# Optimization experiments

Hardware: AMD Instinct MI355X
Metric: run time of the kernel (lower is better)

The kernel has to match this reference:

```python
import jax, jax.numpy as jnp
import numpy as np

B, S, H = 2, 2048, 2048
NH = 16
Q_LORA, KV_LORA = 1536, 512
D_NOPE, D_ROPE, D_V = 128, 64, 128
D_QK = D_NOPE + D_ROPE
SCALE = 1.0 / np.sqrt(D_QK)
EPS = 1e-6


def _freqs(seq_len):
    # precompute_freqs_cis with scaling_factor=1.0 -> plain RoPE
    inv = 1.0 / (10000.0 ** (np.arange(0, D_ROPE, 2, dtype=np.float32) / D_ROPE))
    t = np.arange(seq_len, dtype=np.float32)
    f = np.outer(t, inv)  # (S, D_ROPE//2)
    return jnp.asarray(np.cos(f)), jnp.asarray(np.sin(f))


def _rope_interleaved(x, cos, sin):
    # x: (B, S, heads, D_ROPE); cos/sin: (S, D_ROPE//2)
    b, s, h, d = x.shape
    xr = x.reshape(b, s, h, d // 2, 2)
    e, o = xr[..., 0], xr[..., 1]
    c = cos[None, :, None, :]
    sn = sin[None, :, None, :]
    re = e * c - o * sn
    im = e * sn + o * c
    return jnp.stack([re, im], axis=-1).reshape(b, s, h, d)


def _rmsnorm(x, w):
    xf = x.astype(jnp.float32)
    rms = jnp.sqrt(jnp.mean(xf * xf, axis=-1, keepdims=True) + EPS)
    return (w * (xf / rms)).astype(x.dtype)


def setup_inputs() -> dict:
    key = jax.random.key(0)
    ks = jax.random.split(key, 6)
    def w(k, shape, fan_in):
        return jax.random.normal(k, shape, dtype=jnp.float32) * (1.0 / np.sqrt(fan_in))
    return {
        "hidden_states": jax.random.normal(ks[0], (B, S, H), dtype=jnp.float32),
        "wq_a": w(ks[1], (Q_LORA, H), H),
        "q_norm_w": jnp.ones((Q_LORA,), dtype=jnp.float32),
        "wq_b": w(ks[2], (NH * D_QK, Q_LORA), Q_LORA),
        "wkv_a": w(ks[3], (KV_LORA + D_ROPE, H), H),
        "kv_norm_w": jnp.ones((KV_LORA,), dtype=jnp.float32),
        "wkv_b": w(ks[4], (NH * (D_NOPE + D_V), KV_LORA), KV_LORA),
        "wo": w(ks[5], (H, NH * D_V), NH * D_V),
    }


def reference(hidden_states, wq_a, q_norm_w, wq_b, wkv_a, kv_norm_w, wkv_b, wo):
    b, s, _ = hidden_states.shape
    cos, sin = _freqs(s)

    # low-rank Q path
    q = hidden_states @ wq_a.T                      # (B,S,Q_LORA)
    q = _rmsnorm(q, q_norm_w)
    q = (q @ wq_b.T).reshape(b, s, NH, D_QK)        # (B,S,NH,192)
    q_nope, q_pe = q[..., :D_NOPE], q[..., D_NOPE:]

    # joint KV compression
    kv = hidden_states @ wkv_a.T                    # (B,S,KV_LORA+D_ROPE)
    kv_c, k_pe = kv[..., :KV_LORA], kv[..., KV_LORA:]
    kv_c = _rmsnorm(kv_c, kv_norm_w)
    k_pe = _rope_interleaved(k_pe[:, :, None, :], cos, sin)  # (B,S,1,64)

    kv_x = (kv_c @ wkv_b.T).reshape(b, s, NH, D_NOPE + D_V)
    k_nope, v = kv_x[..., :D_NOPE], kv_x[..., D_NOPE:]

    q_pe = _rope_interleaved(q_pe, cos, sin)
    qf = jnp.concatenate([q_nope, q_pe], axis=-1)   # (B,S,NH,192)
    kf = jnp.concatenate([k_nope, jnp.broadcast_to(k_pe, (b, s, NH, D_ROPE))], axis=-1)

    scores = jnp.einsum("bqhd,bkhd->bhqk", qf, kf) * SCALE
    attn = jax.nn.softmax(scores.astype(jnp.float32), axis=-1).astype(qf.dtype)
    out = jnp.einsum("bhqk,bkhd->bqhd", attn, v).reshape(b, s, NH * D_V)
    return out @ wo.T
```

## Files before the change

### kernel.cpp

```cpp
#include <hip/hip_runtime.h>
#include <math.h>

#define B_   2
#define S_   2048
#define H_   2048
#define NH_  16
#define T_   (B_*S_)
#define QL   1536
#define KVL  512
#define DN   128
#define DR   64
#define DQK  192
#define DV   128
#define SCALE_ 0.07216878364870323f
#define EPS_ 1e-6f

typedef unsigned short u16;
typedef __attribute__((ext_vector_type(8))) short bf16x8;
typedef __attribute__((ext_vector_type(4))) float f32x4;

__device__ __forceinline__ u16 f2b(float x) {
  union { float f; unsigned u; } v; v.f = x;
  unsigned r = v.u + 0x7FFFu + ((v.u >> 16) & 1u);
  return (u16)(r >> 16);
}
__device__ __forceinline__ float b2f(u16 u) {
  union { unsigned u; float f; } v; v.u = ((unsigned)u) << 16; return v.f;
}

#define GLD16(src, dst) __builtin_amdgcn_global_load_lds(                       \
    (const __attribute__((address_space(1))) unsigned int*)(src),               \
    (__attribute__((address_space(3))) unsigned int*)(dst), 16, 0, 0)

__global__ __launch_bounds__(256) void cvt_bf16(const float* __restrict__ in,
                                                u16* __restrict__ out, int n4) {
  int i = blockIdx.x * 256 + threadIdx.x;
  if (i >= n4) return;
  float4 v = ((const float4*)in)[i];
  u16 r[4] = {f2b(v.x), f2b(v.y), f2b(v.z), f2b(v.w)};
  ((uint2*)out)[i] = *(uint2*)r;
}

__global__ __launch_bounds__(256) void cvt_wkva(const float* __restrict__ in,
                                                u16* __restrict__ out) {
  int i = blockIdx.x * 256 + threadIdx.x;
  if (i >= 640 * 512) return;
  int row = i >> 9;
  u16 r[4] = {0, 0, 0, 0};
  if (row < 576) {
    float4 v = ((const float4*)in)[i];
    r[0] = f2b(v.x); r[1] = f2b(v.y); r[2] = f2b(v.z); r[3] = f2b(v.w);
  }
  ((uint2*)out)[i] = *(uint2*)r;
}

template <int OUTMODE>
__global__ __launch_bounds__(256) void gemm_mfma(
    const u16* __restrict__ A, int lda,
    const u16* __restrict__ W, int ldw,
    float* __restrict__ Cf, u16* __restrict__ Cb, int ldc,
    int K, float outscale) {
  __shared__ u16 As[4096];
  __shared__ u16 Bs[4096];
  const int tid = threadIdx.x;
  const int wave = tid >> 6, lane = tid & 63, quad = lane >> 4, l16 = lane & 15;
  const int wm = (wave >> 1) * 64, wn = (wave & 1) * 64;
  const size_t m0 = (size_t)blockIdx.y * 128, n0 = (size_t)blockIdx.x * 128;

  f32x4 acc[4][4];
#pragma unroll
  for (int i = 0; i < 4; ++i)
#pragma unroll
    for (int j = 0; j < 4; ++j) acc[i][j] = (f32x4){0.f, 0.f, 0.f, 0.f};

  const int g0 = tid, g1 = tid + 256;
  const u16* a0 = A + (m0 + (g0 >> 6) * 16 + (g0 & 15)) * (size_t)lda + ((g0 >> 4) & 3) * 8;
  const u16* a1 = A + (m0 + (g1 >> 6) * 16 + (g1 & 15)) * (size_t)lda + ((g1 >> 4) & 3) * 8;
  const u16* b0 = W + (n0 + (g0 >> 6) * 16 + (g0 & 15)) * (size_t)ldw + ((g0 >> 4) & 3) * 8;
  const u16* b1 = W + (n0 + (g1 >> 6) * 16 + (g1 & 15)) * (size_t)ldw + ((g1 >> 4) & 3) * 8;

  for (int k0 = 0; k0 < K; k0 += 32) {
    __syncthreads();
    GLD16(a0 + k0, &As[g0 * 8]);
    GLD16(a1 + k0, &As[g1 * 8]);
    GLD16(b0 + k0, &Bs[g0 * 8]);
    GLD16(b1 + k0, &Bs[g1 * 8]);
    __syncthreads();

    bf16x8 af[4], bfr[4];
#pragma unroll
    for (int i = 0; i < 4; ++i)
      af[i] = *(const bf16x8*)&As[((wm >> 4) + i) * 512 + quad * 128 + l16 * 8];
#pragma unroll
    for (int j = 0; j < 4; ++j)
      bfr[j] = *(const bf16x8*)&Bs[((wn >> 4) + j) * 512 + quad * 128 + l16 * 8];
#pragma unroll
    for (int i = 0; i < 4; ++i)
#pragma unroll
      for (int j = 0; j < 4; ++j)
        acc[i][j] = __builtin_amdgcn_mfma_f32_16x16x32_bf16(af[i], bfr[j], acc[i][j], 0, 0, 0);
  }

#pragma unroll
  for (int i = 0; i < 4; ++i)
#pragma unroll
    for (int j = 0; j < 4; ++j)
#pragma unroll
      for (int r = 0; r < 4; ++r) {
        size_t m = m0 + wm + i * 16 + quad * 4 + r;
        size_t n = n0 + wn + j * 16 + l16;
        if (OUTMODE == 0) Cf[m * ldc + n] = acc[i][j][r];
        else              Cb[m * ldc + n] = f2b(acc[i][j][r] * outscale);
      }
}

__global__ __launch_bounds__(256) void rmsnorm_bf(
    const float* __restrict__ x, const float* __restrict__ w,
    u16* __restrict__ o, int D, int sx, int so) {
  const float* p = x + (size_t)blockIdx.x * sx;
  u16* q = o + (size_t)blockIdx.x * so;
  float ss = 0.f;
  for (int i = threadIdx.x; i < D; i += 256) { float v = p[i]; ss += v * v; }
#pragma unroll
  for (int off = 32; off; off >>= 1) ss += __shfl_down(ss, off);
  __shared__ float red[4];
  __shared__ float s_inv;
  if ((threadIdx.x & 63) == 0) red[threadIdx.x >> 6] = ss;
  __syncthreads();
  if (threadIdx.x == 0) {
    float t = red[0] + red[1] + red[2] + red[3];
    s_inv = 1.0f / sqrtf(t / (float)D + EPS_);
  }
  __syncthreads();
  float inv = s_inv;
  for (int i = threadIdx.x; i < D; i += 256) q[i] = f2b(w[i] * p[i] * inv);
}

__global__ void rope_q_bf(u16* __restrict__ Q) {
  int idx = blockIdx.x * blockDim.x + threadIdx.x;
  int pair = idx & 31;
  int head = (idx >> 5) & (NH_ - 1);
  int row = idx >> 9;
  if (row >= T_) return;
  int s = row & (S_ - 1);
  float inv = powf(10000.0f, -(float)(2 * pair) * (1.0f / 64.0f));
  float ang = (float)s * inv;
  float c = cosf(ang), sn = sinf(ang);
  u16* p = Q + (size_t)row * (NH_ * DQK) + head * DQK + DN + 2 * pair;
  unsigned u = *(unsigned*)p;
  float e = b2f((u16)(u & 0xffff)), o = b2f((u16)(u >> 16));
  float re = e * c - o * sn;
  float im = e * sn + o * c;
  *(unsigned*)p = (unsigned)f2b(re) | ((unsigned)f2b(im) << 16);
}

__global__ void kpe_bf_kernel(const float* __restrict__ KVa, u16* __restrict__ KPE) {
  int idx = blockIdx.x * blockDim.x + threadIdx.x;
  int pair = idx & 31;
  int row = idx >> 5;
  if (row >= T_) return;
  int s = row & (S_ - 1);
  float inv = powf(10000.0f, -(float)(2 * pair) * (1.0f / 64.0f));
  float ang = (float)s * inv;
  float c = cosf(ang), sn = sinf(ang);
  const float* p = KVa + (size_t)row * 640 + KVL + 2 * pair;
  float e = p[0], o = p[1];
  float re = e * c - o * sn;
  float im = e * sn + o * c;
  *(unsigned*)(KPE + (size_t)row * 64 + 2 * pair) =
      (unsigned)f2b(re) | ((unsigned)f2b(im) << 16);
}

__global__ __launch_bounds__(256) void conv_vt(const u16* __restrict__ KVbf,
                                               u16* __restrict__ Vt) {
  const int h = blockIdx.y, b = blockIdx.z;
  const int s0 = (blockIdx.x >> 1) * 64, d0 = (blockIdx.x & 1) * 64;
  const int t0 = b * S_;
  __shared__ u16 tile[64][72];
  const int tid = threadIdx.x;
#pragma unroll
  for (int i = 0; i < 2; ++i) {
    int c = tid + i * 256;
    int row = c >> 3, off = (c & 7) * 8;
    *(uint4*)&tile[row][off] =
        *(const uint4*)(KVbf + (size_t)(t0 + s0 + row) * 4096 + h * 256 + 128 + d0 + off);
  }
  __syncthreads();
#pragma unroll
  for (int i = 0; i < 2; ++i) {
    int c = tid + i * 256;
    int drow = c >> 3, soff = (c & 7) * 8;
    u16 vals[8];
#pragma unroll
    for (int j = 0; j < 8; ++j) vals[j] = tile[soff + j][drow];
    *(uint4*)(Vt + ((size_t)(b * NH_ + h) * 128 + d0 + drow) * 2048 + s0 + soff) =
        *(uint4*)vals;
  }
}

__global__ __launch_bounds__(256) void flash_mfma(
    const u16* __restrict__ Qbf,
    const u16* __restrict__ KVbf,
    const u16* __restrict__ KPE,
    const u16* __restrict__ Vt,
    u16* __restrict__ Out) {
  const int h = blockIdx.y, b = blockIdx.z;
  const int q0 = blockIdx.x * 64;
  const int t0 = b * S_;
  const int tid = threadIdx.x;
  const int wave = tid >> 6, lane = tid & 63, quad = lane >> 4, l16 = lane & 15;

  __shared__ u16 Ks[64][200];
  __shared__ u16 Vs[128][72];
  __shared__ u16 Ps[4][16][72];

  bf16x8 qf[6];
  {
    const u16* qp = Qbf + (size_t)(t0 + q0 + wave * 16 + l16) * (NH_ * DQK) + h * DQK + quad * 8;
#pragma unroll
    for (int c = 0; c < 6; ++c) qf[c] = *(const bf16x8*)(qp + c * 32);
  }

  f32x4 of[8];
#pragma unroll
  for (int i = 0; i < 8; ++i) of[i] = (f32x4){0.f, 0.f, 0.f, 0.f};
  float mrun[4] = {-3e38f, -3e38f, -3e38f, -3e38f};
  float lrun[4] = {0.f, 0.f, 0.f, 0.f};

  for (int kt = 0; kt < S_; kt += 64) {
    __syncthreads();
#pragma unroll
    for (int i = 0; i < 6; ++i) {
      int c = tid + i * 256;
      int row = c / 24, off = c % 24;
      const u16* src = (off < 16)
          ? KVbf + (size_t)(t0 + kt + row) * 4096 + h * 256 + off * 8
          : KPE + (size_t)(t0 + kt + row) * 64 + (off - 16) * 8;
      *(uint4*)&Ks[row][off * 8] = *(const uint4*)src;
    }
#pragma unroll
    for (int i = 0; i < 4; ++i) {
      int c = tid + i * 256;
      int row = c >> 3, off = (c & 7) * 8;
      *(uint4*)&Vs[row][off] =
          *(const uint4*)(Vt + ((size_t)(b * NH_ + h) * 128 + row) * 2048 + kt + off);
    }
    __syncthreads();

    f32x4 sc[4];
#pragma unroll
    for (int kk = 0; kk < 4; ++kk) {
      f32x4 s = (f32x4){0.f, 0.f, 0.f, 0.f};
#pragma unroll
      for (int c = 0; c < 6; ++c) {
        bf16x8 kf = *(const bf16x8*)&Ks[kk * 16 + l16][quad * 8 + c * 32];
        s = __builtin_amdgcn_mfma_f32_16x16x32_bf16(qf[c], kf, s, 0, 0, 0);
      }
      sc[kk] = s;
    }
    float tm[4];
#pragma unroll
    for (int r = 0; r < 4; ++r)
      tm[r] = fmaxf(fmaxf(sc[0][r], sc[1][r]), fmaxf(sc[2][r], sc[3][r]));
#pragma unroll
    for (int off = 1; off < 16; off <<= 1)
#pragma unroll
      for (int r = 0; r < 4; ++r) tm[r] = fmaxf(tm[r], __shfl_xor(tm[r], off, 64));
    float alpha[4], rs[4], p[4][4];
#pragma unroll
    for (int r = 0; r < 4; ++r) {
      float mnew = fmaxf(mrun[r], tm[r]);
      alpha[r] = __expf(mrun[r] - mnew);
      mrun[r] = mnew;
      float s0 = 0.f;
#pragma unroll
      for (int kk = 0; kk < 4; ++kk) {
        float pv = __expf(sc[kk][r] - mnew);
        p[kk][r] = pv;
        s0 += pv;
      }
      rs[r] = s0;
    }
#pragma unroll
    for (int off = 1; off < 16; off <<= 1)
#pragma unroll
      for (int r = 0; r < 4; ++r) rs[r] += __shfl_xor(rs[r], off, 64);
#pragma unroll
    for (int r = 0; r < 4; ++r) lrun[r] = lrun[r] * alpha[r] + rs[r];

#pragma unroll
    for (int kk = 0; kk < 4; ++kk)
#pragma unroll
      for (int r = 0; r < 4; ++r)
        Ps[wave][quad * 4 + r][kk * 16 + l16] = f2b(p[kk][r]);

#pragma unroll
    for (int dt = 0; dt < 8; ++dt)
#pragma unroll
      for (int r = 0; r < 4; ++r) of[dt][r] *= alpha[r];

    bf16x8 pa0 = *(const bf16x8*)&Ps[wave][l16][quad * 8];
    bf16x8 pa1 = *(const bf16x8*)&Ps[wave][l16][32 + quad * 8];
#pragma unroll
    for (int dt = 0; dt < 8; ++dt) {
      bf16x8 v0 = *(const bf16x8*)&Vs[dt * 16 + l16][quad * 8];
      bf16x8 v1 = *(const bf16x8*)&Vs[dt * 16 + l16][32 + quad * 8];
      of[dt] = __builtin_amdgcn_mfma_f32_16x16x32_bf16(pa0, v0, of[dt], 0, 0, 0);
      of[dt] = __builtin_amdgcn_mfma_f32_16x16x32_bf16(pa1, v1, of[dt], 0, 0, 0);
    }
  }

#pragma unroll
  for (int r = 0; r < 4; ++r) {
    float inv = 1.0f / lrun[r];
    u16* op = Out + (size_t)(t0 + q0 + wave * 16 + quad * 4 + r) * (NH_ * DV) + h * DV + l16;
#pragma unroll
    for (int dt = 0; dt < 8; ++dt) op[dt * 16] = f2b(of[dt][r] * inv);
  }
}

extern "C" void kernel_launch(void* const* d_in, const int* in_sizes, int n_in,
                              void* d_out, int out_size, void* d_ws, size_t ws_size,
                              hipStream_t stream) {
  const float* hidden  = (const float*)d_in[0];
  const float* wq_a    = (const float*)d_in[1];
  const float* q_norm  = (const float*)d_in[2];
  const float* wq_b    = (const float*)d_in[3];
  const float* wkv_a   = (const float*)d_in[4];
  const float* kv_norm = (const float*)d_in[5];
  const float* wkv_b   = (const float*)d_in[6];
  const float* wo      = (const float*)d_in[7];
  float* out = (float*)d_out;

  float* ws = (float*)d_ws;
  u16*   hid_bf = (u16*)(ws);
  u16*   wbuf   = (u16*)(ws + 4194304);
  float* q_a    = ws + 6553600;
  u16*   vt     = (u16*)(ws + 6553600);
  u16*   kpe    = (u16*)(ws + 10747904);
  float* kv_a   = ws + 12845056;
  u16*   qn_bf  = (u16*)(ws + 15466496);
  u16*   attn_bf= (u16*)(ws + 15466496);
  u16*   q_bf   = (u16*)(ws + 19660800);
  u16*   kvn_bf = (u16*)(ws + 25952256);
  u16*   kv_bf  = (u16*)(ws + 27000832);
  const size_t need = (size_t)(27000832 + 8388608) * sizeof(float);
  if (ws_size < need) return;

  cvt_bf16<<<8192, 256, 0, stream>>>(hidden, hid_bf, 2097152);

  cvt_bf16<<<3072, 256, 0, stream>>>(wq_a, wbuf, 786432);
  gemm_mfma<0><<<dim3(QL / 128, T_ / 128), 256, 0, stream>>>(
      hid_bf, H_, wbuf, H_, q_a, nullptr, QL, H_, 1.0f);
  rmsnorm_bf<<<T_, 256, 0, stream>>>(q_a, q_norm, qn_bf, QL, QL, QL);
  cvt_bf16<<<4608, 256, 0, stream>>>(wq_b, wbuf, 1179648);
  gemm_mfma<1><<<dim3(NH_ * DQK / 128, T_ / 128), 256, 0, stream>>>(
      qn_bf, QL, wbuf, QL, nullptr, q_bf, NH_ * DQK, QL, SCALE_);
  rope_q_bf<<<T_ * NH_ * 32 / 256, 256, 0, stream>>>(q_bf);

  cvt_wkva<<<1280, 256, 0, stream>>>(wkv_a, wbuf);
  gemm_mfma<0><<<dim3(640 / 128, T_ / 128), 256, 0, stream>>>(
      hid_bf, H_, wbuf, H_, kv_a, nullptr, 640, H_, 1.0f);
  rmsnorm_bf<<<T_, 256, 0, stream>>>(kv_a, kv_norm, kvn_bf, KVL, 640, KVL);
  kpe_bf_kernel<<<T_ * 32 / 256, 256, 0, stream>>>(kv_a, kpe);
  cvt_bf16<<<2048, 256, 0, stream>>>(wkv_b, wbuf, 524288);
  gemm_mfma<1><<<dim3(NH_ * (DN + DV) / 128, T_ / 128), 256, 0, stream>>>(
      kvn_bf, KVL, wbuf, KVL, nullptr, kv_bf, NH_ * (DN + DV), KVL, 1.0f);
  conv_vt<<<dim3(64, NH_, B_), 256, 0, stream>>>(kv_bf, vt);

  flash_mfma<<<dim3(S_ / 64, NH_, B_), 256, 0, stream>>>(q_bf, kv_bf, kpe, vt, attn_bf);

  cvt_bf16<<<4096, 256, 0, stream>>>(wo, wbuf, 1048576);
  gemm_mfma<0><<<dim3(H_ / 128, T_ / 128), 256, 0, stream>>>(
      attn_bf, NH_ * DV, wbuf, NH_ * DV, out, nullptr, H_, NH_ * DV, 1.0f);
}
```

Baseline: 710.2 us.

## Process two query tiles per wave in flash attention with fragment-ordered LDS

Doubles the query rows per block to 128, so each wave handles two 16-row query tiles. Every K and V fragment read from LDS now feeds two MFMAs, which halves per-query K/V staging and LDS read traffic. K, V and P are stored in LDS in MFMA-fragment order rather than padded row-major, and the K/V global load addresses are computed once before the loop and advanced by a stride each iteration. The cost is more accumulator registers (launch bounds ask for 2 blocks per CU) and half as many blocks in the grid.

```diff
diff --git a/kernel.cpp b/kernel.cpp
--- a/kernel.cpp
+++ b/kernel.cpp
@@ -198,125 +198,153 @@
   }
 }
 
-__global__ __launch_bounds__(256) void flash_mfma(
+__global__ __launch_bounds__(256, 2) void flash_mfma(
     const u16* __restrict__ Qbf,
     const u16* __restrict__ KVbf,
     const u16* __restrict__ KPE,
     const u16* __restrict__ Vt,
     u16* __restrict__ Out) {
   const int h = blockIdx.y, b = blockIdx.z;
-  const int q0 = blockIdx.x * 64;
+  const int q0 = blockIdx.x * 128;
   const int t0 = b * S_;
   const int tid = threadIdx.x;
   const int wave = tid >> 6, lane = tid & 63, quad = lane >> 4, l16 = lane & 15;
-
-  __shared__ u16 Ks[64][200];
-  __shared__ u16 Vs[128][72];
-  __shared__ u16 Ps[4][16][72];
-
-  bf16x8 qf[6];
-  {
-    const u16* qp = Qbf + (size_t)(t0 + q0 + wave * 16 + l16) * (NH_ * DQK) + h * DQK + quad * 8;
-#pragma unroll
-    for (int c = 0; c < 6; ++c) qf[c] = *(const bf16x8*)(qp + c * 32);
-  }
-
-  f32x4 of[8];
-#pragma unroll
-  for (int i = 0; i < 8; ++i) of[i] = (f32x4){0.f, 0.f, 0.f, 0.f};
-  float mrun[4] = {-3e38f, -3e38f, -3e38f, -3e38f};
-  float lrun[4] = {0.f, 0.f, 0.f, 0.f};
+  const int wq = wave * 32;
+
+  __shared__ u16 Ks[64 * 192];
+  __shared__ u16 Vs[128 * 64];
+  __shared__ u16 Ps[4][2][16 * 64];
+
+  bf16x8 qf[2][6];
+#pragma unroll
+  for (int t = 0; t < 2; ++t) {
+    const u16* qp = Qbf + (size_t)(t0 + q0 + wq + t * 16 + l16) * (NH_ * DQK) + h * DQK + quad * 8;
+#pragma unroll
+    for (int c = 0; c < 6; ++c) qf[t][c] = *(const bf16x8*)(qp + c * 32);
+  }
+
+  const u16* kbase[6]; int kstep[6];
+#pragma unroll
+  for (int i = 0; i < 6; ++i) {
+    int g = i * 256 + tid;
+    int r = g & 15, cc = (g >> 4) % 24, kk = (g >> 4) / 24;
+    int tok = kk * 16 + r;
+    if (cc < 16) { kbase[i] = KVbf + (size_t)(t0 + tok) * 4096 + h * 256 + cc * 8; kstep[i] = 64 * 4096; }
+    else         { kbase[i] = KPE + (size_t)(t0 + tok) * 64 + (cc - 16) * 8;       kstep[i] = 64 * 64; }
+  }
+  const u16* vbase[4];
+#pragma unroll
+  for (int i = 0; i < 4; ++i) {
+    int g = i * 256 + tid;
+    int r = g & 15, kc = (g >> 4) & 7, dt = g >> 7;
+    vbase[i] = Vt + ((size_t)((b * NH_ + h) * 128) + dt * 16 + r) * 2048 + kc * 8;
+  }
+
+  f32x4 of[2][8];
+#pragma unroll
+  for (int t = 0; t < 2; ++t)
+#pragma unroll
+    for (int i = 0; i < 8; ++i) of[t][i] = (f32x4){0.f, 0.f, 0.f, 0.f};
+  float mrun[2][4], lrun[2][4];
+#pragma unroll
+  for (int t = 0; t < 2; ++t)
+#pragma unroll
+    for (int r = 0; r < 4; ++r) { mrun[t][r] = -3e38f; lrun[t][r] = 0.f; }
 
   for (int kt = 0; kt < S_; kt += 64) {
     __syncthreads();
 #pragma unroll
-    for (int i = 0; i < 6; ++i) {
-      int c = tid + i * 256;
-      int row = c / 24, off = c % 24;
-      const u16* src = (off < 16)
-          ? KVbf + (size_t)(t0 + kt + row) * 4096 + h * 256 + off * 8
-          : KPE + (size_t)(t0 + kt + row) * 64 + (off - 16) * 8;
-      *(uint4*)&Ks[row][off * 8] = *(const uint4*)src;
+    for (int i = 0; i < 6; ++i) GLD16(kbase[i], &Ks[(i * 256 + tid) * 8]);
+#pragma unroll
+    for (int i = 0; i < 4; ++i) GLD16(vbase[i] + kt, &Vs[(i * 256 + tid) * 8]);
+#pragma unroll
+    for (int i = 0; i < 6; ++i) kbase[i] += kstep[i];
+    __syncthreads();
+
+    f32x4 sc[2][4];
+#pragma unroll
+    for (int kk = 0; kk < 4; ++kk) {
+      sc[0][kk] = (f32x4){0.f, 0.f, 0.f, 0.f};
+      sc[1][kk] = (f32x4){0.f, 0.f, 0.f, 0.f};
+#pragma unroll
+      for (int c = 0; c < 6; ++c) {
+        bf16x8 kf = *(const bf16x8*)&Ks[(kk * 384 + (c * 4 + quad) * 16 + l16) * 8];
+        sc[0][kk] = __builtin_amdgcn_mfma_f32_16x16x32_bf16(qf[0][c], kf, sc[0][kk], 0, 0, 0);
+        sc[1][kk] = __builtin_amdgcn_mfma_f32_16x16x32_bf16(qf[1][c], kf, sc[1][kk], 0, 0, 0);
+      }
     }
-#pragma unroll
-    for (int i = 0; i < 4; ++i) {
-      int c = tid + i * 256;
-      int row = c >> 3, off = (c & 7) * 8;
-      *(uint4*)&Vs[row][off] =
-          *(const uint4*)(Vt + ((size_t)(b * NH_ + h) * 128 + row) * 2048 + kt + off);
+
+    float alpha[2][4];
+#pragma unroll
+    for (int t = 0; t < 2; ++t) {
+      float tm[4], rs[4];
+#pragma unroll
+      for (int r = 0; r < 4; ++r)
+        tm[r] = fmaxf(fmaxf(sc[t][0][r], sc[t][1][r]), fmaxf(sc[t][2][r], sc[t][3][r]));
+#pragma unroll
+      for (int off = 1; off < 16; off <<= 1)
+#pragma unroll
+        for (int r = 0; r < 4; ++r) tm[r] = fmaxf(tm[r], __shfl_xor(tm[r], off, 64));
+#pragma unroll
+      for (int r = 0; r < 4; ++r) {
+        float mnew = fmaxf(mrun[t][r], tm[r]);
+        alpha[t][r] = __expf(mrun[t][r] - mnew);
+        mrun[t][r] = mnew;
+        float s0 = 0.f;
+#pragma unroll
+        for (int kk = 0; kk < 4; ++kk) {
+          float pv = __expf(sc[t][kk][r] - mnew);
+          sc[t][kk][r] = pv;
+          s0 += pv;
+        }
+        rs[r] = s0;
+      }
+#pragma unroll
+      for (int off = 1; off < 16; off <<= 1)
+#pragma unroll
+        for (int r = 0; r < 4; ++r) rs[r] += __shfl_xor(rs[r], off, 64);
+#pragma unroll
+      for (int r = 0; r < 4; ++r) lrun[t][r] = lrun[t][r] * alpha[t][r] + rs[r];
+#pragma unroll
+      for (int kk = 0; kk < 4; ++kk)
+#pragma unroll
+        for (int r = 0; r < 4; ++r)
+          Ps[wave][t][((kk * 2 + (l16 >> 3)) * 16 + quad * 4 + r) * 8 + (l16 & 7)] =
+              f2b(sc[t][kk][r]);
     }
-    __syncthreads();
-
-    f32x4 sc[4];
-#pragma unroll
-    for (int kk = 0; kk < 4; ++kk) {
-      f32x4 s = (f32x4){0.f, 0.f, 0.f, 0.f};
-#pragma unroll
-      for (int c = 0; c < 6; ++c) {
-        bf16x8 kf = *(const bf16x8*)&Ks[kk * 16 + l16][quad * 8 + c * 32];
-        s = __builtin_amdgcn_mfma_f32_16x16x32_bf16(qf[c], kf, s, 0, 0, 0);
+
+    bf16x8 pa[2][2];
+#pragma unroll
+    for (int t = 0; t < 2; ++t)
+#pragma unroll
+      for (int c2 = 0; c2 < 2; ++c2)
+        pa[t][c2] = *(const bf16x8*)&Ps[wave][t][((c2 * 4 + quad) * 16 + l16) * 8];
+#pragma unroll
+    for (int t = 0; t < 2; ++t)
+#pragma unroll
+      for (int dt = 0; dt < 8; ++dt)
+#pragma unroll
+        for (int r = 0; r < 4; ++r) of[t][dt][r] *= alpha[t][r];
+#pragma unroll
+    for (int dt = 0; dt < 8; ++dt) {
+#pragma unroll
+      for (int c2 = 0; c2 < 2; ++c2) {
+        bf16x8 vf = *(const bf16x8*)&Vs[(dt * 128 + (c2 * 4 + quad) * 16 + l16) * 8];
+        of[0][dt] = __builtin_amdgcn_mfma_f32_16x16x32_bf16(pa[0][c2], vf, of[0][dt], 0, 0, 0);
+        of[1][dt] = __builtin_amdgcn_mfma_f32_16x16x32_bf16(pa[1][c2], vf, of[1][dt], 0, 0, 0);
       }
-      sc[kk] = s;
     }
-    float tm[4];
-#pragma unroll
-    for (int r = 0; r < 4; ++r)
-      tm[r] = fmaxf(fmaxf(sc[0][r], sc[1][r]), fmaxf(sc[2][r], sc[3][r]));
-#pragma unroll
-    for (int off = 1; off < 16; off <<= 1)
-#pragma unroll
-      for (int r = 0; r < 4; ++r) tm[r] = fmaxf(tm[r], __shfl_xor(tm[r], off, 64));
-    float alpha[4], rs[4], p[4][4];
+  }
+
+#pragma unroll
+  for (int t = 0; t < 2; ++t)
 #pragma unroll
     for (int r = 0; r < 4; ++r) {
-      float mnew = fmaxf(mrun[r], tm[r]);
-      alpha[r] = __expf(mrun[r] - mnew);
-      mrun[r] = mnew;
-      float s0 = 0.f;
-#pragma unroll
-      for (int kk = 0; kk < 4; ++kk) {
-        float pv = __expf(sc[kk][r] - mnew);
-        p[kk][r] = pv;
-        s0 += pv;
-      }
-      rs[r] = s0;
+      float inv = 1.0f / lrun[t][r];
+      u16* op = Out + (size_t)(t0 + q0 + wq + t * 16 + quad * 4 + r) * (NH_ * DV) + h * DV + l16;
+#pragma unroll
+      for (int dt = 0; dt < 8; ++dt) op[dt * 16] = f2b(of[t][dt][r] * inv);
     }
-#pragma unroll
-    for (int off = 1; off < 16; off <<= 1)
-#pragma unroll
-      for (int r = 0; r < 4; ++r) rs[r] += __shfl_xor(rs[r], off, 64);
-#pragma unroll
-    for (int r = 0; r < 4; ++r) lrun[r] = lrun[r] * alpha[r] + rs[r];
-
-#pragma unroll
-    for (int kk = 0; kk < 4; ++kk)
-#pragma unroll
-      for (int r = 0; r < 4; ++r)
-        Ps[wave][quad * 4 + r][kk * 16 + l16] = f2b(p[kk][r]);
-
-#pragma unroll
-    for (int dt = 0; dt < 8; ++dt)
-#pragma unroll
-      for (int r = 0; r < 4; ++r) of[dt][r] *= alpha[r];
-
-    bf16x8 pa0 = *(const bf16x8*)&Ps[wave][l16][quad * 8];
-    bf16x8 pa1 = *(const bf16x8*)&Ps[wave][l16][32 + quad * 8];
-#pragma unroll
-    for (int dt = 0; dt < 8; ++dt) {
-      bf16x8 v0 = *(const bf16x8*)&Vs[dt * 16 + l16][quad * 8];
-      bf16x8 v1 = *(const bf16x8*)&Vs[dt * 16 + l16][32 + quad * 8];
-      of[dt] = __builtin_amdgcn_mfma_f32_16x16x32_bf16(pa0, v0, of[dt], 0, 0, 0);
-      of[dt] = __builtin_amdgcn_mfma_f32_16x16x32_bf16(pa1, v1, of[dt], 0, 0, 0);
-    }
-  }
-
-#pragma unroll
-  for (int r = 0; r < 4; ++r) {
-    float inv = 1.0f / lrun[r];
-    u16* op = Out + (size_t)(t0 + q0 + wave * 16 + quad * 4 + r) * (NH_ * DV) + h * DV + l16;
-#pragma unroll
-    for (int dt = 0; dt < 8; ++dt) op[dt * 16] = f2b(of[dt][r] * inv);
-  }
 }
 
 extern "C" void kernel_launch(void* const* d_in, const int* in_sizes, int n_in,
@@ -368,7 +396,7 @@
       kvn_bf, KVL, wbuf, KVL, nullptr, kv_bf, NH_ * (DN + DV), KVL, 1.0f);
   conv_vt<<<dim3(64, NH_, B_), 256, 0, stream>>>(kv_bf, vt);
 
-  flash_mfma<<<dim3(S_ / 64, NH_, B_), 256, 0, stream>>>(q_bf, kv_bf, kpe, vt, attn_bf);
+  flash_mfma<<<dim3(S_ / 128, NH_, B_), 256, 0, stream>>>(q_bf, kv_bf, kpe, vt, attn_bf);
 
   cvt_bf16<<<4096, 256, 0, stream>>>(wo, wbuf, 1048576);
   gemm_mfma<0><<<dim3(H_ / 128, T_ / 128), 256, 0, stream>>>(
```

New measurement: 677.9 us. 1.05x faster.

## Fuse fp32-to-bf16 conversions and use async LDS loads in flash attention

Applied to the files above, without the earlier changes.

All six fp32-to-bf16 conversions are merged into one launch, and the workspace is reorganised so each converted weight gets its own buffer instead of sharing one. The flash attention kernel moves to 512-thread blocks covering 128 queries. K and V tiles are loaded with global_load_lds directly into a fragment-ordered LDS layout, and the P scratch reuses the K buffer behind an extra barrier. The aim is fewer launches, fewer K/V tile reloads per head, and cheaper tile staging. The cost is an added __syncthreads per iteration and a larger workspace.

```diff
diff --git a/kernel.cpp b/kernel.cpp
--- a/kernel.cpp
+++ b/kernel.cpp
@@ -32,26 +32,39 @@
     (const __attribute__((address_space(1))) unsigned int*)(src),               \
     (__attribute__((address_space(3))) unsigned int*)(dst), 16, 0, 0)
 
-__global__ __launch_bounds__(256) void cvt_bf16(const float* __restrict__ in,
-                                                u16* __restrict__ out, int n4) {
-  int i = blockIdx.x * 256 + threadIdx.x;
-  if (i >= n4) return;
+__device__ __forceinline__ void cvt4(const float* in, u16* out, int i) {
   float4 v = ((const float4*)in)[i];
   u16 r[4] = {f2b(v.x), f2b(v.y), f2b(v.z), f2b(v.w)};
   ((uint2*)out)[i] = *(uint2*)r;
 }
 
-__global__ __launch_bounds__(256) void cvt_wkva(const float* __restrict__ in,
-                                                u16* __restrict__ out) {
+__global__ __launch_bounds__(256) void cvt_all(
+    const float* __restrict__ hid, const float* __restrict__ wqa,
+    const float* __restrict__ wqb, const float* __restrict__ wkva,
+    const float* __restrict__ wkvb, const float* __restrict__ wo,
+    u16* __restrict__ o_hid, u16* __restrict__ o_wqa, u16* __restrict__ o_wqb,
+    u16* __restrict__ o_wkva, u16* __restrict__ o_wkvb, u16* __restrict__ o_wo) {
   int i = blockIdx.x * 256 + threadIdx.x;
-  if (i >= 640 * 512) return;
-  int row = i >> 9;
-  u16 r[4] = {0, 0, 0, 0};
-  if (row < 576) {
-    float4 v = ((const float4*)in)[i];
-    r[0] = f2b(v.x); r[1] = f2b(v.y); r[2] = f2b(v.z); r[3] = f2b(v.w);
-  }
-  ((uint2*)out)[i] = *(uint2*)r;
+  if (i < 2097152) { cvt4(hid, o_hid, i); return; }
+  i -= 2097152;
+  if (i < 786432) { cvt4(wqa, o_wqa, i); return; }
+  i -= 786432;
+  if (i < 1179648) { cvt4(wqb, o_wqb, i); return; }
+  i -= 1179648;
+  if (i < 327680) {
+    int row = i >> 9;
+    u16 r[4] = {0, 0, 0, 0};
+    if (row < 576) {
+      float4 v = ((const float4*)wkva)[i];
+      r[0] = f2b(v.x); r[1] = f2b(v.y); r[2] = f2b(v.z); r[3] = f2b(v.w);
+    }
+    ((uint2*)o_wkva)[i] = *(uint2*)r;
+    return;
+  }
+  i -= 327680;
+  if (i < 524288) { cvt4(wkvb, o_wkvb, i); return; }
+  i -= 524288;
+  if (i < 1048576) cvt4(wo, o_wo, i);
 }
 
 template <int OUTMODE>
@@ -198,21 +211,21 @@
   }
 }
 
-__global__ __launch_bounds__(256) void flash_mfma(
+__global__ __launch_bounds__(512, 4) void flash_mfma(
     const u16* __restrict__ Qbf,
     const u16* __restrict__ KVbf,
     const u16* __restrict__ KPE,
     const u16* __restrict__ Vt,
     u16* __restrict__ Out) {
   const int h = blockIdx.y, b = blockIdx.z;
-  const int q0 = blockIdx.x * 64;
+  const int q0 = blockIdx.x * 128;
   const int t0 = b * S_;
   const int tid = threadIdx.x;
   const int wave = tid >> 6, lane = tid & 63, quad = lane >> 4, l16 = lane & 15;
 
-  __shared__ u16 Ks[64][200];
-  __shared__ u16 Vs[128][72];
-  __shared__ u16 Ps[4][16][72];
+  __shared__ u16 Ks[64 * 192];
+  __shared__ u16 Vs[128 * 64];
+  u16* Ps = &Ks[wave * 1024];
 
   bf16x8 qf[6];
   {
@@ -221,6 +234,23 @@
     for (int c = 0; c < 6; ++c) qf[c] = *(const bf16x8*)(qp + c * 32);
   }
 
+  const u16* kbase[3]; int kstep[3];
+#pragma unroll
+  for (int i = 0; i < 3; ++i) {
+    int g = i * 512 + tid;
+    int r = g & 15, cc = (g >> 4) % 24, kk = (g >> 4) / 24;
+    int tok = kk * 16 + r;
+    if (cc < 16) { kbase[i] = KVbf + (size_t)(t0 + tok) * 4096 + h * 256 + cc * 8; kstep[i] = 64 * 4096; }
+    else         { kbase[i] = KPE + (size_t)(t0 + tok) * 64 + (cc - 16) * 8;       kstep[i] = 64 * 64; }
+  }
+  const u16* vbase[2];
+#pragma unroll
+  for (int i = 0; i < 2; ++i) {
+    int g = i * 512 + tid;
+    int r = g & 15, kc = (g >> 4) & 7, dt = g >> 7;
+    vbase[i] = Vt + ((size_t)((b * NH_ + h) * 128) + dt * 16 + r) * 2048 + kc * 8;
+  }
+
   f32x4 of[8];
 #pragma unroll
   for (int i = 0; i < 8; ++i) of[i] = (f32x4){0.f, 0.f, 0.f, 0.f};
@@ -230,21 +260,11 @@
   for (int kt = 0; kt < S_; kt += 64) {
     __syncthreads();
 #pragma unroll
-    for (int i = 0; i < 6; ++i) {
-      int c = tid + i * 256;
-      int row = c / 24, off = c % 24;
-      const u16* src = (off < 16)
-          ? KVbf + (size_t)(t0 + kt + row) * 4096 + h * 256 + off * 8
-          : KPE + (size_t)(t0 + kt + row) * 64 + (off - 16) * 8;
-      *(uint4*)&Ks[row][off * 8] = *(const uint4*)src;
-    }
-#pragma unroll
-    for (int i = 0; i < 4; ++i) {
-      int c = tid + i * 256;
-      int row = c >> 3, off = (c & 7) * 8;
-      *(uint4*)&Vs[row][off] =
-          *(const uint4*)(Vt + ((size_t)(b * NH_ + h) * 128 + row) * 2048 + kt + off);
-    }
+    for (int i = 0; i < 3; ++i) GLD16(kbase[i], &Ks[(i * 512 + tid) * 8]);
+#pragma unroll
+    for (int i = 0; i < 2; ++i) GLD16(vbase[i] + kt, &Vs[(i * 512 + tid) * 8]);
+#pragma unroll
+    for (int i = 0; i < 3; ++i) kbase[i] += kstep[i];
     __syncthreads();
 
     f32x4 sc[4];
@@ -253,12 +273,13 @@
       f32x4 s = (f32x4){0.f, 0.f, 0.f, 0.f};
 #pragma unroll
       for (int c = 0; c < 6; ++c) {
-        bf16x8 kf = *(const bf16x8*)&Ks[kk * 16 + l16][quad * 8 + c * 32];
+        bf16x8 kf = *(const bf16x8*)&Ks[((kk * 24 + c * 4 + quad) * 16 + l16) * 8];
         s = __builtin_amdgcn_mfma_f32_16x16x32_bf16(qf[c], kf, s, 0, 0, 0);
       }
       sc[kk] = s;
     }
-    float tm[4];
+
+    float tm[4], rs[4], alpha[4];
 #pragma unroll
     for (int r = 0; r < 4; ++r)
       tm[r] = fmaxf(fmaxf(sc[0][r], sc[1][r]), fmaxf(sc[2][r], sc[3][r]));
@@ -266,7 +287,6 @@
     for (int off = 1; off < 16; off <<= 1)
 #pragma unroll
       for (int r = 0; r < 4; ++r) tm[r] = fmaxf(tm[r], __shfl_xor(tm[r], off, 64));
-    float alpha[4], rs[4], p[4][4];
 #pragma unroll
     for (int r = 0; r < 4; ++r) {
       float mnew = fmaxf(mrun[r], tm[r]);
@@ -276,7 +296,7 @@
 #pragma unroll
       for (int kk = 0; kk < 4; ++kk) {
         float pv = __expf(sc[kk][r] - mnew);
-        p[kk][r] = pv;
+        sc[kk][r] = pv;
         s0 += pv;
       }
       rs[r] = s0;
@@ -288,25 +308,30 @@
 #pragma unroll
     for (int r = 0; r < 4; ++r) lrun[r] = lrun[r] * alpha[r] + rs[r];
 
+    __syncthreads();
+
 #pragma unroll
     for (int kk = 0; kk < 4; ++kk)
 #pragma unroll
       for (int r = 0; r < 4; ++r)
-        Ps[wave][quad * 4 + r][kk * 16 + l16] = f2b(p[kk][r]);
+        Ps[((kk * 2 + (l16 >> 3)) * 16 + quad * 4 + r) * 8 + (l16 & 7)] = f2b(sc[kk][r]);
 
 #pragma unroll
     for (int dt = 0; dt < 8; ++dt)
 #pragma unroll
       for (int r = 0; r < 4; ++r) of[dt][r] *= alpha[r];
 
-    bf16x8 pa0 = *(const bf16x8*)&Ps[wave][l16][quad * 8];
-    bf16x8 pa1 = *(const bf16x8*)&Ps[wave][l16][32 + quad * 8];
+    bf16x8 pa[2];
+#pragma unroll
+    for (int c2 = 0; c2 < 2; ++c2)
+      pa[c2] = *(const bf16x8*)&Ps[((c2 * 4 + quad) * 16 + l16) * 8];
 #pragma unroll
     for (int dt = 0; dt < 8; ++dt) {
-      bf16x8 v0 = *(const bf16x8*)&Vs[dt * 16 + l16][quad * 8];
-      bf16x8 v1 = *(const bf16x8*)&Vs[dt * 16 + l16][32 + quad * 8];
-      of[dt] = __builtin_amdgcn_mfma_f32_16x16x32_bf16(pa0, v0, of[dt], 0, 0, 0);
-      of[dt] = __builtin_amdgcn_mfma_f32_16x16x32_bf16(pa1, v1, of[dt], 0, 0, 0);
+#pragma unroll
+      for (int c2 = 0; c2 < 2; ++c2) {
+        bf16x8 vf = *(const bf16x8*)&Vs[((dt * 8 + c2 * 4 + quad) * 16 + l16) * 8];
+        of[dt] = __builtin_amdgcn_mfma_f32_16x16x32_bf16(pa[c2], vf, of[dt], 0, 0, 0);
+      }
     }
   }
 
@@ -333,44 +358,44 @@
   float* out = (float*)d_out;
 
   float* ws = (float*)d_ws;
-  u16*   hid_bf = (u16*)(ws);
-  u16*   wbuf   = (u16*)(ws + 4194304);
-  float* q_a    = ws + 6553600;
-  u16*   vt     = (u16*)(ws + 6553600);
-  u16*   kpe    = (u16*)(ws + 10747904);
-  float* kv_a   = ws + 12845056;
-  u16*   qn_bf  = (u16*)(ws + 15466496);
-  u16*   attn_bf= (u16*)(ws + 15466496);
-  u16*   q_bf   = (u16*)(ws + 19660800);
-  u16*   kvn_bf = (u16*)(ws + 25952256);
-  u16*   kv_bf  = (u16*)(ws + 27000832);
-  const size_t need = (size_t)(27000832 + 8388608) * sizeof(float);
+  u16*   hid_bf  = (u16*)(ws);
+  u16*   wqa_bf  = (u16*)(ws + 4194304);
+  u16*   wqb_bf  = (u16*)(ws + 5767168);
+  u16*   wkva_bf = (u16*)(ws + 8126464);
+  u16*   wkvb_bf = (u16*)(ws + 8781824);
+  u16*   wo_bf   = (u16*)(ws + 9830400);
+  float* q_a     = ws + 11927552;
+  u16*   attn_bf = (u16*)(ws + 11927552);
+  u16*   qn_bf   = (u16*)(ws + 18219008);
+  u16*   vt      = (u16*)(ws + 18219008);
+  float* kv_a    = ws + 19791872;
+  u16*   q_bf    = (u16*)(ws + 22413312);
+  u16*   kvn_bf  = (u16*)(ws + 28704768);
+  u16*   kpe     = (u16*)(ws + 29753344);
+  u16*   kv_bf   = (u16*)(ws + 29884416);
+  const size_t need = (size_t)38273024 * sizeof(float);
   if (ws_size < need) return;
 
-  cvt_bf16<<<8192, 256, 0, stream>>>(hidden, hid_bf, 2097152);
-
-  cvt_bf16<<<3072, 256, 0, stream>>>(wq_a, wbuf, 786432);
+  cvt_all<<<23296, 256, 0, stream>>>(hidden, wq_a, wq_b, wkv_a, wkv_b, wo,
+                                     hid_bf, wqa_bf, wqb_bf, wkva_bf, wkvb_bf, wo_bf);
+
   gemm_mfma<0><<<dim3(QL / 128, T_ / 128), 256, 0, stream>>>(
-      hid_bf, H_, wbuf, H_, q_a, nullptr, QL, H_, 1.0f);
+      hid_bf, H_, wqa_bf, H_, q_a, nullptr, QL, H_, 1.0f);
   rmsnorm_bf<<<T_, 256, 0, stream>>>(q_a, q_norm, qn_bf, QL, QL, QL);
-  cvt_bf16<<<4608, 256, 0, stream>>>(wq_b, wbuf, 1179648);
   gemm_mfma<1><<<dim3(NH_ * DQK / 128, T_ / 128), 256, 0, stream>>>(
-      qn_bf, QL, wbuf, QL, nullptr, q_bf, NH_ * DQK, QL, SCALE_);
+      qn_bf, QL, wqb_bf, QL, nullptr, q_bf, NH_ * DQK, QL, SCALE_);
   rope_q_bf<<<T_ * NH_ * 32 / 256, 256, 0, stream>>>(q_bf);
 
-  cvt_wkva<<<1280, 256, 0, stream>>>(wkv_a, wbuf);
   gemm_mfma<0><<<dim3(640 / 128, T_ / 128), 256, 0, stream>>>(
-      hid_bf, H_, wbuf, H_, kv_a, nullptr, 640, H_, 1.0f);
+      hid_bf, H_, wkva_bf, H_, kv_a, nullptr, 640, H_, 1.0f);
   rmsnorm_bf<<<T_, 256, 0, stream>>>(kv_a, kv_norm, kvn_bf, KVL, 640, KVL);
   kpe_bf_kernel<<<T_ * 32 / 256, 256, 0, stream>>>(kv_a, kpe);
-  cvt_bf16<<<2048, 256, 0, stream>>>(wkv_b, wbuf, 524288);
   gemm_mfma<1><<<dim3(NH_ * (DN + DV) / 128, T_ / 128), 256, 0, stream>>>(
-      kvn_bf, KVL, wbuf, KVL, nullptr, kv_bf, NH_ * (DN + DV), KVL, 1.0f);
+      kvn_bf, KVL, wkvb_bf, KVL, nullptr, kv_bf, NH_ * (DN + DV), KVL, 1.0f);
   conv_vt<<<dim3(64, NH_, B_), 256, 0, stream>>>(kv_bf, vt);
 
-  flash_mfma<<<dim3(S_ / 64, NH_, B_), 256, 0, stream>>>(q_bf, kv_bf, kpe, vt, attn_bf);
-
-  cvt_bf16<<<4096, 256, 0, stream>>>(wo, wbuf, 1048576);
+  flash_mfma<<<dim3(S_ / 128, NH_, B_), 512, 0, stream>>>(q_bf, kv_bf, kpe, vt, attn_bf);
+
   gemm_mfma<0><<<dim3(H_ / 128, T_ / 128), 256, 0, stream>>>(
-      attn_bf, NH_ * DV, wbuf, NH_ * DV, out, nullptr, H_, NH_ * DV, 1.0f);
-}
+      attn_bf, NH_ * DV, wo_bf, NH_ * DV, out, nullptr, H_, NH_ * DV, 1.0f);
+}
```

Measured after the change: 651.6 us. 8.2% less time.
